# Kernel tuning notes

Hardware: AMD Instinct MI355X
Metric: run time of the kernel (lower is better)

Reference implementation:

```python
import jax, jax.numpy as jnp
import numpy as np

NUM_CLASSES = 2
TOP_K = 1500
CONF_THRESH = 0.01
NMS_THRESH = 0.2
VAR0, VAR1 = 0.1, 0.2  # cfg['variance']


def setup_inputs() -> dict:
    key = jax.random.key(0)
    k1, k2, k3 = jax.random.split(key, 3)
    B, P = 32, 76800
    loc_data = jax.random.normal(k1, (B, P, 4), jnp.float32)
    conf_data = jax.random.uniform(k2, (B * P, NUM_CLASSES), jnp.float32)
    prior_data = jax.random.uniform(k3, (P, 4), jnp.float32)
    return {"loc_data": loc_data, "conf_data": conf_data, "prior_data": prior_data}


def _decode(loc, priors):
    # loc, priors: [P,4]; SSD box decode with variances
    cxcy = priors[:, :2] + loc[:, :2] * VAR0 * priors[:, 2:]
    wh = priors[:, 2:] * jnp.exp(loc[:, 2:] * VAR1)
    x1y1 = cxcy - wh * 0.5
    return jnp.concatenate([x1y1, x1y1 + wh], axis=-1)  # [P,4] (x1,y1,x2,y2)


def _nms_per_class(scores, boxes):
    # scores: [P], boxes: [P,4] -> [TOP_K,5] packed (score,x1,y1,x2,y2)
    s = jnp.where(scores > CONF_THRESH, scores, -jnp.inf)
    sk, idx = jax.lax.top_k(s, TOP_K)  # torch nms keeps only top_k candidates
    bk = boxes[idx]
    x1, y1, x2, y2 = bk[:, 0], bk[:, 1], bk[:, 2], bk[:, 3]
    area = (x2 - x1) * (y2 - y1)
    iota = jnp.arange(TOP_K)

    def step(active, i):
        # greedy NMS over score-descending candidates
        xx1 = jnp.maximum(x1, x1[i]); yy1 = jnp.maximum(y1, y1[i])
        xx2 = jnp.minimum(x2, x2[i]); yy2 = jnp.minimum(y2, y2[i])
        inter = jnp.maximum(xx2 - xx1, 0.0) * jnp.maximum(yy2 - yy1, 0.0)
        iou = inter / (area + area[i] - inter)
        kept = active[i]
        suppress = (iou > NMS_THRESH) & (iota != i)
        active = jnp.where(kept, active & ~suppress, active)
        return active, kept

    _, keep = jax.lax.scan(step, sk > -jnp.inf, iota)
    rows = jnp.where(keep[:, None], jnp.concatenate([sk[:, None], bk], axis=1), 0.0)
    # pack kept rows at the front (score-descending order), zeros after
    rank = jnp.cumsum(keep) - 1
    dest = jnp.where(keep, rank, TOP_K)  # dump non-kept into scratch slot
    return jnp.zeros((TOP_K + 1, 5), bk.dtype).at[dest].set(rows)[:TOP_K]


def reference(loc_data, conf_data, prior_data):
    B, P, _ = loc_data.shape
    conf = conf_data.reshape(B, P, NUM_CLASSES)
    decoded = jax.vmap(_decode, in_axes=(0, None))(loc_data, prior_data)  # [B,P,4]
    outs = []
    for cl in range(1, NUM_CLASSES):  # background class 0 stays zero
        outs.append(jax.vmap(_nms_per_class)(conf[:, :, cl], decoded))
    bg = jnp.zeros((B, 1, TOP_K, 5), decoded.dtype)
    return jnp.concatenate([bg, jnp.stack(outs, axis=1)], axis=1)  # [B,C,TOP_K,5]
```

## Files before the change

### kernel.cpp

```cpp
#include <hip/hip_runtime.h>
#include <stdint.h>

typedef unsigned long long u64;
typedef unsigned int u32;

#define NUM_B 32
#define NUM_P 76800
#define TOPK 1500
#define NBINS 4096
#define CAP 2048
#define NWORDS 24
#define NCHUNK 6
#define CPAD 32
#define HSLICES 8
#define HCHUNK (NUM_P / HSLICES)

__device__ __forceinline__ u32 fbits(float f) { return __float_as_uint(f); }
__device__ __forceinline__ int binOf(float s) {
    int b = (int)(s * (float)NBINS);
    return (b > NBINS - 1) ? NBINS - 1 : b;
}
__device__ __forceinline__ u64 readlane64(u64 v, int l) {
    u32 lo = (u32)__builtin_amdgcn_readlane((int)(u32)(v & 0xffffffffu), l);
    u32 hi = (u32)__builtin_amdgcn_readlane((int)(u32)(v >> 32), l);
    return ((u64)hi << 32) | lo;
}

__global__ void zero_kernel(u32* a, int n, u32* c, int nc, u32* d, int nd) {
    int i = blockIdx.x * blockDim.x + threadIdx.x;
    int stride = gridDim.x * blockDim.x;
    for (int t = i; t < n; t += stride) a[t] = 0;
    for (int t = i; t < nc; t += stride) c[t] = 0;
    for (int t = i; t < nd; t += stride) d[t] = 0;
}

__global__ __launch_bounds__(256) void hist_kernel(const float4* __restrict__ conf4,
                                                   u32* __restrict__ hist) {
    int c = blockIdx.x, b = blockIdx.y, tid = threadIdx.x;
    __shared__ u32 h[NBINS];
    for (int i = tid; i < NBINS; i += 256) h[i] = 0;
    __syncthreads();
    const float4* base = conf4 + (size_t)b * (NUM_P / 2) + (size_t)c * (HCHUNK / 2);
    for (int i = tid; i < HCHUNK / 2; i += 256) {
        float4 v = base[i];
        if (v.y > 0.01f) atomicAdd(&h[binOf(v.y)], 1u);
        if (v.w > 0.01f) atomicAdd(&h[binOf(v.w)], 1u);
    }
    __syncthreads();
    u32* outp = hist + ((size_t)b * HSLICES + c) * NBINS;
    for (int i = tid; i < NBINS; i += 256) outp[i] = h[i];
}

__global__ void thresh_kernel(const u32* __restrict__ hist, int* __restrict__ tbin) {
    int b = blockIdx.x;
    int tid = threadIdx.x;
    const u32* hb = hist + (size_t)b * HSLICES * NBINS;
    __shared__ u32 vals[256];
    __shared__ int s_min;
    u32 total = 0;
    for (int c = 0; c < NBINS / 256; ++c) {
        if (tid == 0) s_min = 256;
        int bin = NBINS - 1 - (c * 256 + tid);
        u32 v = 0;
#pragma unroll
        for (int s = 0; s < HSLICES; ++s) v += hb[(size_t)s * NBINS + bin];
        __syncthreads();
        vals[tid] = v;
        __syncthreads();
        for (int off = 1; off < 256; off <<= 1) {
            u32 add = (tid >= off) ? vals[tid - off] : 0;
            __syncthreads();
            vals[tid] += add;
            __syncthreads();
        }
        u32 cum = total + vals[tid];
        if (cum >= TOPK) atomicMin(&s_min, tid);
        __syncthreads();
        if (s_min < 256) {
            if (tid == 0) tbin[b] = NBINS - 1 - (c * 256 + s_min);
            return;
        }
        total += vals[255];
    }
    if (tid == 0) tbin[b] = 0;
}

__global__ __launch_bounds__(256) void compact_kernel(
    const float4* __restrict__ conf4, const int* __restrict__ tbin,
    u32* __restrict__ counts, u64* __restrict__ keys) {
    int b = blockIdx.y;
    int tid = threadIdx.x;
    int lane = tid & 63, wave = tid >> 6;
    int f4 = blockIdx.x * 256 + tid;
    float4 c = conf4[(size_t)b * (NUM_P / 2) + f4];
    int tb = tbin[b];
    int p0 = f4 * 2, p1 = p0 + 1;
    bool v0 = (c.y > 0.01f) && (binOf(c.y) >= tb);
    bool v1 = (c.w > 0.01f) && (binOf(c.w) >= tb);

    u64 m0 = __ballot(v0), m1 = __ballot(v1);
    u32 c0 = (u32)__popcll(m0);
    u64 below = (1ULL << lane) - 1ULL;
    u32 off0 = (u32)__popcll(m0 & below);
    u32 off1 = c0 + (u32)__popcll(m1 & below);
    u32 wtot = c0 + (u32)__popcll(m1);

    __shared__ u32 wcnt[4];
    __shared__ u32 s_base;
    if (lane == 0) wcnt[wave] = wtot;
    __syncthreads();
    if (tid == 0) {
        u32 tot = wcnt[0] + wcnt[1] + wcnt[2] + wcnt[3];
        s_base = (tot > 0) ? atomicAdd(&counts[(size_t)b * CPAD], tot) : 0u;
    }
    __syncthreads();
    u32 woff = 0;
    for (int w = 0; w < wave; ++w) woff += wcnt[w];
    if (v0) {
        u32 pos = s_base + woff + off0;
        if (pos < CAP) keys[(size_t)b * CAP + pos] = ((u64)fbits(c.y) << 32) | (u32)(~p0);
    }
    if (v1) {
        u32 pos = s_base + woff + off1;
        if (pos < CAP) keys[(size_t)b * CAP + pos] = ((u64)fbits(c.w) << 32) | (u32)(~p1);
    }
}

__global__ __launch_bounds__(256) void rank_decode_kernel(
    const u64* __restrict__ keys, const u32* __restrict__ counts,
    const float* __restrict__ loc, const float* __restrict__ prior,
    float* __restrict__ sscore, float* __restrict__ sbox) {
#pragma clang fp contract(off)
    int blk = blockIdx.x, b = blockIdx.y, tid = threadIdx.x;
    __shared__ u64 k[CAP];
    int n = (int)min(counts[(size_t)b * CPAD], (u32)CAP);
    for (int t = tid; t < CAP; t += 256)
        k[t] = (t < n) ? keys[(size_t)b * CAP + t] : 0ULL;
    __syncthreads();

    int t = blk * 256 + tid;
    u64 mykey = k[t];
    if (mykey == 0ULL) return;

    u32 rank = 0;
#pragma unroll 8
    for (int j = 0; j < CAP; ++j) rank += (k[j] > mykey) ? 1u : 0u;

    if (rank < TOPK) {
        u32 pidx = ~(u32)mykey;
        float sc = __uint_as_float((u32)(mykey >> 32));
        const float* lp = &loc[((size_t)b * NUM_P + pidx) * 4];
        const float* pp = &prior[(size_t)pidx * 4];
        float lx = lp[0], ly = lp[1], lw = lp[2], lh = lp[3];
        float pcx = pp[0], pcy = pp[1], pw = pp[2], ph = pp[3];
        float cx = pcx + (lx * 0.1f) * pw;
        float cy = pcy + (ly * 0.1f) * ph;
        float w  = pw * expf(lw * 0.2f);
        float h  = ph * expf(lh * 0.2f);
        float x1 = cx - w * 0.5f;
        float y1 = cy - h * 0.5f;
        float x2 = x1 + w;
        float y2 = y1 + h;
        sscore[(size_t)b * TOPK + rank] = sc;
        float* bx = &sbox[((size_t)b * TOPK + rank) * 4];
        bx[0] = x1; bx[1] = y1; bx[2] = x2; bx[3] = y2;
    }
}

__global__ __launch_bounds__(256) void mask_kernel(
    const float* __restrict__ sbox, u64* __restrict__ mask) {
#pragma clang fp contract(off)
    int w = blockIdx.x, c = blockIdx.y, b = blockIdx.z, tid = threadIdx.x;
    int i = c * 256 + tid;
    __shared__ float4 cbox[64];
    __shared__ float car[64];
    bool blk_live = (w * 64 + 63) > (c * 256);
    if (blk_live) {
        if (tid < 64) {
            int j = w * 64 + tid;
            float4 bx = make_float4(0.f, 0.f, 0.f, 0.f);
            if (j < TOPK) bx = ((const float4*)sbox)[(size_t)b * TOPK + j];
            cbox[tid] = bx;
            car[tid] = (bx.z - bx.x) * (bx.w - bx.y);
        }
        __syncthreads();
    }
    u64 m = 0;
    if (blk_live && i < TOPK && (w * 64 + 63) > i) {
        const double MID = 0.5 * ((double)__uint_as_float(0x3E4CCCCDu) +
                                  (double)__uint_as_float(0x3E4CCCCEu));
        const float4 bx = ((const float4*)sbox)[(size_t)b * TOPK + i];
        float x1i = bx.x, y1i = bx.y, x2i = bx.z, y2i = bx.w;
        float ai = (x2i - x1i) * (y2i - y1i);
        u64 jmask = (i < w * 64) ? ~0ULL : (~0ULL << (i - w * 64 + 1));
        for (int j2 = 0; j2 < 64; ++j2) {
            float4 cb = cbox[j2];
            float xx1 = fmaxf(cb.x, x1i);
            float yy1 = fmaxf(cb.y, y1i);
            float xx2 = fminf(cb.z, x2i);
            float yy2 = fminf(cb.w, y2i);
            float iw = fmaxf(xx2 - xx1, 0.0f);
            float ih = fmaxf(yy2 - yy1, 0.0f);
            float inter = iw * ih;
            float denom = (car[j2] + ai) - inter;
            if ((double)inter >= MID * (double)denom) m |= (1ULL << j2);
        }
        m &= jmask;
    }
    if (i < TOPK)
        mask[((size_t)b * NWORDS + w) * TOPK + i] = m;
}

__global__ __launch_bounds__(256) void sweep_kernel(
    const u64* __restrict__ mask, const float* __restrict__ sscore,
    const float* __restrict__ sbox, float* __restrict__ out) {
    int b = blockIdx.x, tid = threadIdx.x;
    int lane = tid & 63, wid = tid >> 6;

    const u64* mbase = mask + (size_t)b * NWORDS * TOPK;

    __shared__ u64 rowbuf[3][NWORDS][65];
    __shared__ u64 aw[NWORDS];
    __shared__ u32 pfx[NWORDS + 1];

    u64 act = 0;
    u64 sv[8];
    if (wid == 0) {
        for (int c = 0; c < NWORDS; ++c) {
            int r = c * 64 + lane;
            bool v = (r < TOPK) && (sscore[(size_t)b * TOPK + r] > 0.0f);
            u64 m = __ballot(v);
            if (lane == c) act = m;
        }
    } else {
        int w0 = (wid - 1) * 8;
#pragma unroll
        for (int t = 0; t < 2; ++t) {
            u64 tmp[8];
#pragma unroll
            for (int k = 0; k < 8; ++k)
                tmp[k] = mbase[(size_t)(w0 + k) * TOPK + t * 64 + lane];
#pragma unroll
            for (int k = 0; k < 8; ++k)
                rowbuf[t][w0 + k][lane] = tmp[k];
        }
        {
            int rr = 2 * 64 + lane;
#pragma unroll
            for (int k = 0; k < 8; ++k)
                sv[k] = mbase[(size_t)(w0 + k) * TOPK + rr];
        }
    }
    __syncthreads();

    for (int T = 0; T < NWORDS; ++T) {
        if (wid == 0) {
            u64 dreg = rowbuf[T % 3][T][lane];
            u64 actw = readlane64(act, T);
            u64 kept = 0, rem = actw;
            while (rem) {
                int i2 = __ffsll(rem) - 1;
                kept |= (1ULL << i2);
                rem &= rem - 1;
                rem &= ~readlane64(dreg, i2);
            }
            if (lane == T) act = kept;
            if (lane > T && lane < NWORDS) {
                u64 kb = kept;
                while (kb) {
                    int r = __ffsll(kb) - 1;
                    kb &= kb - 1;
                    act &= ~rowbuf[T % 3][lane][r];
                }
            }
        } else {
            int tw = T + 2;
            if (tw < NWORDS) {
                int w0 = (wid - 1) * 8;
#pragma unroll
                for (int k = 0; k < 8; ++k)
                    rowbuf[tw % 3][w0 + k][lane] = sv[k];
                int tn = T + 3;
                if (tn < NWORDS) {
                    int rr = tn * 64 + lane;
                    bool vr = rr < TOPK;
#pragma unroll
                    for (int k = 0; k < 8; ++k)
                        sv[k] = vr ? mbase[(size_t)(w0 + k) * TOPK + rr] : 0ULL;
                }
            }
        }
        __syncthreads();
    }

    if (wid == 0 && lane < NWORDS) aw[lane] = act;
    __syncthreads();
    if (tid == 0) {
        u32 acc = 0;
        for (int wd = 0; wd < NWORDS; ++wd) { pfx[wd] = acc; acc += (u32)__popcll(aw[wd]); }
        pfx[NWORDS] = acc;
    }
    __syncthreads();
    for (int r = tid; r < TOPK; r += 256) {
        int wd = r >> 6;
        u64 word = aw[wd];
        if ((word >> (r & 63)) & 1ULL) {
            u32 rank = pfx[wd] + (u32)__popcll(word & ((1ULL << (r & 63)) - 1ULL));
            float sc = sscore[(size_t)b * TOPK + r];
            float4 bx = ((const float4*)sbox)[(size_t)b * TOPK + r];
            size_t base_o = (((size_t)b * 2 + 1) * TOPK + (size_t)rank) * 5;
            out[base_o + 0] = sc;
            out[base_o + 1] = bx.x;
            out[base_o + 2] = bx.y;
            out[base_o + 3] = bx.z;
            out[base_o + 4] = bx.w;
        }
    }
}

extern "C" void kernel_launch(void* const* d_in, const int* in_sizes, int n_in,
                              void* d_out, int out_size, void* d_ws, size_t ws_size,
                              hipStream_t stream) {
    const float* loc   = (const float*)d_in[0];
    const float* conf  = (const float*)d_in[1];
    const float* prior = (const float*)d_in[2];
    float* out = (float*)d_out;
    char* ws = (char*)d_ws;

    u64* mask_buf = (u64*)(ws + 0);
    u32* hist     = (u32*)(ws + 0);
    u64* keys     = (u64*)(ws + 4194304);
    u32* counts   = (u32*)(ws + 4718592);
    int* tbin     = (int*)(ws + 4722688);
    float* sscore = (float*)(ws + 9216000);
    float* sbox   = (float*)(ws + 9408000);

    zero_kernel<<<512, 256, 0, stream>>>(counts, NUM_B * CPAD, (u32*)out, 480000,
                                         (u32*)sscore, 240000);
    hist_kernel<<<dim3(HSLICES, 32), 256, 0, stream>>>((const float4*)conf, hist);
    thresh_kernel<<<32, 256, 0, stream>>>(hist, tbin);
    compact_kernel<<<dim3(150, 32), 256, 0, stream>>>((const float4*)conf, tbin, counts, keys);
    rank_decode_kernel<<<dim3(CAP / 256, 32), 256, 0, stream>>>(keys, counts, loc, prior,
                                                                sscore, sbox);
    mask_kernel<<<dim3(NWORDS, NCHUNK, 32), 256, 0, stream>>>(sbox, mask_buf);
    sweep_kernel<<<32, 256, 0, stream>>>(mask_buf, sscore, sbox, out);
}
```

Before: 197.9 us.

## Remove zero kernel, fold zeroing into hist and sweep, double hist slices

Drops the separate zeroing launch: the counts reset moves into hist_kernel and output zeroing moves into sweep_kernel, while the sscore zeroing is removed entirely. Histogram slices go from 8 to 16 to give more blocks, and the workspace offsets shift to fit the larger histogram. mask_kernel now exits early for dead blocks and no longer writes zero words for them, and sweep skips loading those below-diagonal mask words. The risk is that sscore entries past the compacted count are no longer cleared, and the sweep relies on them being zero.

```diff
diff --git a/kernel.cpp b/kernel.cpp
--- a/kernel.cpp
+++ b/kernel.cpp
@@ -12,7 +12,7 @@
 #define NWORDS 24
 #define NCHUNK 6
 #define CPAD 32
-#define HSLICES 8
+#define HSLICES 16
 #define HCHUNK (NUM_P / HSLICES)
 
 __device__ __forceinline__ u32 fbits(float f) { return __float_as_uint(f); }
@@ -26,17 +26,11 @@
     return ((u64)hi << 32) | lo;
 }
 
-__global__ void zero_kernel(u32* a, int n, u32* c, int nc, u32* d, int nd) {
-    int i = blockIdx.x * blockDim.x + threadIdx.x;
-    int stride = gridDim.x * blockDim.x;
-    for (int t = i; t < n; t += stride) a[t] = 0;
-    for (int t = i; t < nc; t += stride) c[t] = 0;
-    for (int t = i; t < nd; t += stride) d[t] = 0;
-}
-
 __global__ __launch_bounds__(256) void hist_kernel(const float4* __restrict__ conf4,
-                                                   u32* __restrict__ hist) {
+                                                   u32* __restrict__ hist,
+                                                   u32* __restrict__ counts) {
     int c = blockIdx.x, b = blockIdx.y, tid = threadIdx.x;
+    if (c == 0 && tid < CPAD) counts[(size_t)b * CPAD + tid] = 0;
     __shared__ u32 h[NBINS];
     for (int i = tid; i < NBINS; i += 256) h[i] = 0;
     __syncthreads();
@@ -172,27 +166,25 @@
 #pragma clang fp contract(off)
     int w = blockIdx.x, c = blockIdx.y, b = blockIdx.z, tid = threadIdx.x;
     int i = c * 256 + tid;
+    if ((w * 64 + 63) <= (c * 256)) return;
     __shared__ float4 cbox[64];
     __shared__ float car[64];
-    bool blk_live = (w * 64 + 63) > (c * 256);
-    if (blk_live) {
-        if (tid < 64) {
-            int j = w * 64 + tid;
-            float4 bx = make_float4(0.f, 0.f, 0.f, 0.f);
-            if (j < TOPK) bx = ((const float4*)sbox)[(size_t)b * TOPK + j];
-            cbox[tid] = bx;
-            car[tid] = (bx.z - bx.x) * (bx.w - bx.y);
-        }
-        __syncthreads();
-    }
-    u64 m = 0;
-    if (blk_live && i < TOPK && (w * 64 + 63) > i) {
+    if (tid < 64) {
+        int j = w * 64 + tid;
+        float4 bx = make_float4(0.f, 0.f, 0.f, 0.f);
+        if (j < TOPK) bx = ((const float4*)sbox)[(size_t)b * TOPK + j];
+        cbox[tid] = bx;
+        car[tid] = (bx.z - bx.x) * (bx.w - bx.y);
+    }
+    __syncthreads();
+    if (i < TOPK && (w * 64 + 63) > i) {
         const double MID = 0.5 * ((double)__uint_as_float(0x3E4CCCCDu) +
                                   (double)__uint_as_float(0x3E4CCCCEu));
         const float4 bx = ((const float4*)sbox)[(size_t)b * TOPK + i];
         float x1i = bx.x, y1i = bx.y, x2i = bx.z, y2i = bx.w;
         float ai = (x2i - x1i) * (y2i - y1i);
         u64 jmask = (i < w * 64) ? ~0ULL : (~0ULL << (i - w * 64 + 1));
+        u64 m = 0;
         for (int j2 = 0; j2 < 64; ++j2) {
             float4 cb = cbox[j2];
             float xx1 = fmaxf(cb.x, x1i);
@@ -206,9 +198,8 @@
             if ((double)inter >= MID * (double)denom) m |= (1ULL << j2);
         }
         m &= jmask;
-    }
-    if (i < TOPK)
         mask[((size_t)b * NWORDS + w) * TOPK + i] = m;
+    }
 }
 
 __global__ __launch_bounds__(256) void sweep_kernel(
@@ -239,7 +230,7 @@
             u64 tmp[8];
 #pragma unroll
             for (int k = 0; k < 8; ++k)
-                tmp[k] = mbase[(size_t)(w0 + k) * TOPK + t * 64 + lane];
+                tmp[k] = (w0 + k >= t) ? mbase[(size_t)(w0 + k) * TOPK + t * 64 + lane] : 0ULL;
 #pragma unroll
             for (int k = 0; k < 8; ++k)
                 rowbuf[t][w0 + k][lane] = tmp[k];
@@ -248,7 +239,7 @@
             int rr = 2 * 64 + lane;
 #pragma unroll
             for (int k = 0; k < 8; ++k)
-                sv[k] = mbase[(size_t)(w0 + k) * TOPK + rr];
+                sv[k] = (w0 + k >= 2) ? mbase[(size_t)(w0 + k) * TOPK + rr] : 0ULL;
         }
     }
     __syncthreads();
@@ -286,7 +277,8 @@
                     bool vr = rr < TOPK;
 #pragma unroll
                     for (int k = 0; k < 8; ++k)
-                        sv[k] = vr ? mbase[(size_t)(w0 + k) * TOPK + rr] : 0ULL;
+                        sv[k] = (vr && (w0 + k >= tn))
+                                    ? mbase[(size_t)(w0 + k) * TOPK + rr] : 0ULL;
                 }
             }
         }
@@ -294,6 +286,11 @@
     }
 
     if (wid == 0 && lane < NWORDS) aw[lane] = act;
+    {
+        float* p0 = out + ((size_t)b * 2 + 0) * TOPK * 5;
+        float* p1 = out + ((size_t)b * 2 + 1) * TOPK * 5;
+        for (int t = tid; t < TOPK * 5; t += 256) { p0[t] = 0.0f; p1[t] = 0.0f; }
+    }
     __syncthreads();
     if (tid == 0) {
         u32 acc = 0;
@@ -329,15 +326,13 @@
 
     u64* mask_buf = (u64*)(ws + 0);
     u32* hist     = (u32*)(ws + 0);
-    u64* keys     = (u64*)(ws + 4194304);
-    u32* counts   = (u32*)(ws + 4718592);
-    int* tbin     = (int*)(ws + 4722688);
+    u64* keys     = (u64*)(ws + 8388608);
+    u32* counts   = (u32*)(ws + 8912896);
+    int* tbin     = (int*)(ws + 8916992);
     float* sscore = (float*)(ws + 9216000);
     float* sbox   = (float*)(ws + 9408000);
 
-    zero_kernel<<<512, 256, 0, stream>>>(counts, NUM_B * CPAD, (u32*)out, 480000,
-                                         (u32*)sscore, 240000);
-    hist_kernel<<<dim3(HSLICES, 32), 256, 0, stream>>>((const float4*)conf, hist);
+    hist_kernel<<<dim3(HSLICES, 32), 256, 0, stream>>>((const float4*)conf, hist, counts);
     thresh_kernel<<<32, 256, 0, stream>>>(hist, tbin);
     compact_kernel<<<dim3(150, 32), 256, 0, stream>>>((const float4*)conf, tbin, counts, keys);
     rank_decode_kernel<<<dim3(CAP / 256, 32), 256, 0, stream>>>(keys, counts, loc, prior,
```

Measured after the change: 194.3 us, median of 2. No clear change (-1.8%).
